# Performance work log

Hardware: AMD Instinct MI355X
Metric: run time of the kernel (lower is better)

The kernel has to match this reference:

```python
import jax, jax.numpy as jnp
import numpy as np

B, L_IN, D_MODEL, CONV_D, KSIZE = 16, 512, 384, 1536, 3
MEL_MAX = 4096
LN_EPS = 1e-5


def _conv1d_same(h, w, b):
    # h: [B, C_in, L], w: [C_out, C_in, K] -> [B, C_out, L]
    y = jax.lax.conv_general_dilated(h, w, window_strides=(1,), padding='SAME',
                                     dimension_numbers=('NCH', 'OIH', 'NCH'))
    return y + b[None, :, None]


def _layernorm(x, g, b):
    m = jnp.mean(x, -1, keepdims=True)
    v = jnp.mean((x - m) ** 2, -1, keepdims=True)
    return (x - m) * jax.lax.rsqrt(v + LN_EPS) * g + b


def _ffn(x, wa, ba, wb, bb):
    # Conv1D_FFT: conv(d_model->conv_d) ReLU conv(conv_d->d_model) ReLU
    h = jnp.transpose(x, (0, 2, 1))
    h = jax.nn.relu(_conv1d_same(h, wa, ba))
    h = jax.nn.relu(_conv1d_same(h, wb, bb))
    return jnp.transpose(h, (0, 2, 1))


def _dur_pred(x, w1, b1, w2, b2, g1, be1, w3, b3, w4, b4, g2, be2, wl, bl):
    h = _ffn(x, w1, b1, w2, b2)
    h = _layernorm(h, g1, be1)  # dropout is identity at eval
    h = _ffn(h, w3, b3, w4, b4)
    h = _layernorm(h, g2, be2)
    return (h @ wl + bl)[..., 0]  # [B, L_in], squeeze(-1)


def _length_regulate(x, dur, mel_max_len):
    # Equivalent to alignment @ x where alignment[b,t,j]=1 iff cum[b,j-1] <= t < cum[b,j],
    # padded with zeros out to mel_max_len (original pads output to mel_max_len).
    cum = jnp.cumsum(dur, axis=-1)                        # [B, L_in]
    total = cum[:, -1]                                    # [B]
    t = jnp.arange(mel_max_len, dtype=cum.dtype)          # [T]
    idx = jax.vmap(lambda c: jnp.searchsorted(c, t, side='right'))(cum)  # [B, T]
    idx = jnp.minimum(idx, x.shape[1] - 1)
    out = jnp.take_along_axis(x, idx[:, :, None], axis=1)  # [B, T, D]
    mask = (t[None, :] < total[:, None])[..., None]
    return out * mask


def setup_inputs() -> dict:
    key = jax.random.key(0)
    ks = jax.random.split(key, 8)
    def nrm(k, shape):
        return jax.random.normal(k, shape, jnp.float32) * 0.02
    return {
        'x': jax.random.normal(ks[0], (B, L_IN, D_MODEL), jnp.float32),
        'target': jax.random.randint(ks[1], (B, L_IN), 0, 8, jnp.int32),
        'mel_max_len': MEL_MAX,
        'w1': nrm(ks[2], (CONV_D, D_MODEL, KSIZE)), 'b1': jnp.zeros((CONV_D,), jnp.float32),
        'w2': nrm(ks[3], (D_MODEL, CONV_D, KSIZE)), 'b2': jnp.zeros((D_MODEL,), jnp.float32),
        'g1': jnp.ones((D_MODEL,), jnp.float32), 'be1': jnp.zeros((D_MODEL,), jnp.float32),
        'w3': nrm(ks[4], (CONV_D, D_MODEL, KSIZE)), 'b3': jnp.zeros((CONV_D,), jnp.float32),
        'w4': nrm(ks[5], (D_MODEL, CONV_D, KSIZE)), 'b4': jnp.zeros((D_MODEL,), jnp.float32),
        'g2': jnp.ones((D_MODEL,), jnp.float32), 'be2': jnp.zeros((D_MODEL,), jnp.float32),
        'wl': nrm(ks[6], (D_MODEL, 1)), 'bl': jnp.zeros((1,), jnp.float32),
    }


def reference(x, target, mel_max_len, w1, b1, w2, b2, g1, be1, w3, b3, w4, b4, g2, be2, wl, bl):
    dur_preds = _dur_pred(x, w1, b1, w2, b2, g1, be1, w3, b3, w4, b4, g2, be2, wl, bl)
    output = _length_regulate(x, target, mel_max_len)
    return (output, dur_preds)
```

## Files before the change

### kernel.cpp

```cpp
#include <hip/hip_runtime.h>
#include <hip/hip_bf16.h>
#include <cstddef>
#include <cstdint>

#define NB 16
#define LIN 512
#define DM 384
#define DC 1536
#define MELMAX 4096
#define LN_EPS 1e-5f

typedef __bf16 bf16x8 __attribute__((ext_vector_type(8)));
typedef float f32x4 __attribute__((ext_vector_type(4)));

#define GL2LDS(gp, lp)                                                                \
    __builtin_amdgcn_global_load_lds((const __attribute__((address_space(1))) void*)(gp), \
                                     (__attribute__((address_space(3))) void*)(lp), 16, 0, 0)

__device__ __forceinline__ float wred(float v) {
#pragma unroll
    for (int m = 32; m >= 1; m >>= 1) v += __shfl_xor(v, m, 64);
    return v;
}

__device__ __forceinline__ unsigned short f2bf(float f) {
    __hip_bfloat16 h = __float2bfloat16(f);
    return *reinterpret_cast<unsigned short*>(&h);
}

__device__ __forceinline__ float bf2f(unsigned short u) {
    return __uint_as_float(((unsigned)u) << 16);
}


__global__ void cumsum_kernel(const int* __restrict__ tgt, int* __restrict__ cum) {
    __shared__ int s[LIN];
    const int b = blockIdx.x, tid = threadIdx.x;
    s[tid] = tgt[b * LIN + tid];
    __syncthreads();
    for (int off = 1; off < LIN; off <<= 1) {
        int v = (tid >= off) ? s[tid - off] : 0;
        __syncthreads();
        s[tid] += v;
        __syncthreads();
    }
    cum[b * LIN + tid] = s[tid];
}


__global__ __launch_bounds__(256) void gather_kernel(const float* __restrict__ x,
                                                     const int* __restrict__ cum,
                                                     float* __restrict__ out) {
    const int wid = (blockIdx.x * 256 + threadIdx.x) >> 6;
    const int lane = threadIdx.x & 63;
    const int b = wid >> 12;
    const int t = wid & (MELMAX - 1);
    const int* c = cum + b * LIN;
    const int total = c[LIN - 1];
    float4* orow = reinterpret_cast<float4*>(out + ((size_t)b * MELMAX + t) * DM);
    if (t < total) {
        int lo = 0, hi = LIN;
        while (lo < hi) { int mid = (lo + hi) >> 1; if (c[mid] > t) hi = mid; else lo = mid + 1; }
        const int idx = lo < (LIN - 1) ? lo : (LIN - 1);
        const float4* xrow = reinterpret_cast<const float4*>(x + ((size_t)b * LIN + idx) * DM);
#pragma unroll
        for (int j = 0; j < 2; ++j) {
            const int p = lane + 64 * j;
            if (p < DM / 4) orow[p] = xrow[p];
        }
    } else {
        const float4 z = make_float4(0.f, 0.f, 0.f, 0.f);
#pragma unroll
        for (int j = 0; j < 2; ++j) {
            const int p = lane + 64 * j;
            if (p < DM / 4) orow[p] = z;
        }
    }
}


__global__ void zpad3_kernel(unsigned short* __restrict__ xb, unsigned short* __restrict__ hb,
                             unsigned short* __restrict__ h2) {
    const int i = blockIdx.x;
    const int buf = i >> 5, rem = i & 31;
    const int b = rem >> 1, row = (rem & 1) ? (LIN + 1) : 0;
    unsigned short* p = buf == 0 ? xb : (buf == 1 ? hb : h2);
    const int rl = buf == 1 ? DC : DM;
    unsigned short* base = p + ((size_t)b * (LIN + 2) + row) * rl;
    for (int c = threadIdx.x; c < rl; c += 256) base[c] = 0;
}

__global__ void cast_x_kernel(const float* __restrict__ x, unsigned short* __restrict__ xb) {
    const int idx = blockIdx.x * 256 + threadIdx.x;
    const int total = NB * LIN * DM / 4;
    if (idx >= total) return;
    const float4 v = reinterpret_cast<const float4*>(x)[idx];
    const int e = idx * 4;
    const int b = e / (LIN * DM);
    const int rem = e - b * (LIN * DM);
    const int l = rem / DM;
    const int c = rem - l * DM;
    ushort4 o;
    o.x = f2bf(v.x); o.y = f2bf(v.y); o.z = f2bf(v.z); o.w = f2bf(v.w);
    *reinterpret_cast<ushort4*>(xb + ((size_t)b * (LIN + 2) + l + 1) * DM + c) = o;
}

__global__ void wcast_all_kernel(const float* __restrict__ w1, const float* __restrict__ w2,
                                 const float* __restrict__ w3, const float* __restrict__ w4,
                                 unsigned short* __restrict__ o1, unsigned short* __restrict__ o2,
                                 unsigned short* __restrict__ o3, unsigned short* __restrict__ o4) {
    const int idx = blockIdx.x * 256 + threadIdx.x;
    if (idx >= DC * DM) return;
    const int which = blockIdx.y;
    const float* w = which == 0 ? w1 : which == 1 ? w2 : which == 2 ? w3 : w4;
    unsigned short* gg = which == 0 ? o1 : which == 1 ? o2 : which == 2 ? o3 : o4;
    const int CI = (which == 0 || which == 2) ? DM : DC;
    const int co = idx / CI, ci = idx - co * CI;
    const float* p = w + (size_t)idx * 3;
    unsigned short* o = gg + (size_t)co * (3 * CI) + ci;
    o[0 * CI] = f2bf(p[0]);
    o[1 * CI] = f2bf(p[1]);
    o[2 * CI] = f2bf(p[2]);
}


template <int CI, int CO, int BN>
__global__ __launch_bounds__(256, 2) void conv_mfma_kernel(const unsigned short* __restrict__ in,
                                                           const unsigned short* __restrict__ wg,
                                                           const float* __restrict__ bias,
                                                           unsigned short* __restrict__ out) {
    constexpr int BM = 128, BK = 32;
    constexpr int KC = CI / BK;
    constexpr int AROWS = BM + 16;
    constexpr int AGRP = AROWS / 16;
    constexpr int GPT = BN / 16;
    constexpr int BGRP = 3 * GPT;
    constexpr int NW_N = BN / 32;
    constexpr int NT = CO / BN;
    constexpr int MT = LIN / BM;

    __shared__ __align__(16) unsigned short As[2][AROWS * BK];
    __shared__ __align__(16) unsigned short Bs[2][3 * BN * BK];

    const int orig = blockIdx.x, nwg = gridDim.x;
    const int q = nwg >> 3, r = nwg & 7, xcd = orig & 7, o = orig >> 3;
    const int wgid = (xcd < r ? xcd * (q + 1) : r * (q + 1) + (xcd - r) * q) + o;

    const int mg = wgid / NT;
    const int nt = wgid - mg * NT;
    const int b = mg >> 2;
    const int l0 = (mg & (MT - 1)) * BM;
    const int n0 = nt * BN;

    const int tid = threadIdx.x;
    const int lane = tid & 63;
    const int wv = tid >> 6;
    const int wr = wv >> 1, wc = wv & 1;

    const unsigned short* inb = in + (size_t)b * (LIN + 2) * CI;

    f32x4 acc[4][NW_N];
#pragma unroll
    for (int m = 0; m < 4; ++m)
#pragma unroll
        for (int n = 0; n < NW_N; ++n) acc[m][n] = (f32x4){0.f, 0.f, 0.f, 0.f};

    const int lrow = lane >> 2;
    const int lch = lane & 3;
    const int fr = lane & 15, kg = lane >> 4;

    const unsigned short* aroot = inb + (size_t)l0 * CI + lch * 8;
    const unsigned short* broot = wg + (size_t)n0 * (3 * CI) + lch * 8;

#define STAGE(c, kb)                                                                      \
    do {                                                                                  \
        const unsigned short* abase = aroot + (kb) * BK;                                  \
        for (int g = wv; g < AGRP; g += 4)                                                \
            GL2LDS(abase + (size_t)(g * 16 + lrow) * CI, &As[c][g * 512]);                \
        const unsigned short* bbase = broot + (kb) * BK;                                  \
        for (int g2 = wv; g2 < BGRP; g2 += 4) {                                           \
            const int t = g2 / GPT, gr = g2 - t * GPT;                                    \
            GL2LDS(bbase + (size_t)(gr * 16 + lrow) * (3 * CI) + (size_t)t * CI,          \
                   &Bs[c][g2 * 512]);                                                     \
        }                                                                                 \
    } while (0)

#define COMPUTE(c)                                                                        \
    do {                                                                                  \
        _Pragma("unroll")                                                                 \
        for (int t = 0; t < 3; ++t) {                                                     \
            bf16x8 aF[4], bF[NW_N];                                                       \
            _Pragma("unroll")                                                             \
            for (int m = 0; m < 4; ++m)                                                   \
                aF[m] = *reinterpret_cast<const bf16x8*>(                                 \
                    &As[c][(t + wr * 64 + m * 16 + fr) * BK + kg * 8]);                   \
            _Pragma("unroll")                                                             \
            for (int n = 0; n < NW_N; ++n)                                                \
                bF[n] = *reinterpret_cast<const bf16x8*>(                                 \
                    &Bs[c][(t * BN + wc * (BN / 2) + n * 16 + fr) * BK + kg * 8]);        \
            _Pragma("unroll")                                                             \
            for (int m = 0; m < 4; ++m)                                                   \
                _Pragma("unroll")                                                         \
                for (int n = 0; n < NW_N; ++n)                                            \
                    acc[m][n] =                                                           \
                        __builtin_amdgcn_mfma_f32_16x16x32_bf16(aF[m], bF[n], acc[m][n],  \
                                                                0, 0, 0);                 \
        }                                                                                 \
    } while (0)

    STAGE(0, 0);
    __syncthreads();
#pragma unroll 1
    for (int kb = 0; kb < KC; kb += 2) {
        if (kb + 1 < KC) STAGE(1, kb + 1);
        COMPUTE(0);
        __syncthreads();
        if (kb + 2 < KC) STAGE(0, kb + 2);
        if (kb + 1 < KC) {
            COMPUTE(1);
            __syncthreads();
        }
    }
#undef STAGE
#undef COMPUTE

    const int fq = lane >> 4;
    float bv[NW_N];
#pragma unroll
    for (int n = 0; n < NW_N; ++n) bv[n] = bias[n0 + wc * (BN / 2) + n * 16 + fr];
    unsigned short* outb = out + (size_t)b * (LIN + 2) * CO;
#pragma unroll
    for (int m = 0; m < 4; ++m)
#pragma unroll
        for (int qy = 0; qy < 4; ++qy) {
            const int grow = l0 + wr * 64 + m * 16 + fq * 4 + qy + 1;
            unsigned short* orow = outb + (size_t)grow * CO + n0 + wc * (BN / 2) + fr;
#pragma unroll
            for (int n = 0; n < NW_N; ++n) {
                const float v = fmaxf(acc[m][n][qy] + bv[n], 0.f);
                orow[n * 16] = f2bf(v);
            }
        }
}


__global__ void ln_kernel(unsigned short* __restrict__ h, const float* __restrict__ g,
                          const float* __restrict__ be) {
    const int row = blockIdx.x, lane = threadIdx.x;
    const int b = row >> 9, l = row & (LIN - 1);
    unsigned short* hr = h + ((size_t)b * (LIN + 2) + l + 1) * DM;
    float v[6];
    float s = 0.f;
#pragma unroll
    for (int j = 0; j < 6; ++j) { v[j] = bf2f(hr[lane + 64 * j]); s += v[j]; }
    s = wred(s);
    const float mean = s * (1.f / DM);
    float vs = 0.f;
#pragma unroll
    for (int j = 0; j < 6; ++j) { const float d = v[j] - mean; vs += d * d; }
    vs = wred(vs);
    const float rstd = rsqrtf(vs * (1.f / DM) + LN_EPS);
#pragma unroll
    for (int j = 0; j < 6; ++j) {
        const int c = lane + 64 * j;
        hr[c] = f2bf((v[j] - mean) * rstd * g[c] + be[c]);
    }
}


__global__ void ln_linear_kernel(const unsigned short* __restrict__ h, const float* __restrict__ g,
                                 const float* __restrict__ be, const float* __restrict__ wl,
                                 const float* __restrict__ bl, float* __restrict__ dur) {
    const int row = blockIdx.x, lane = threadIdx.x;
    const int b = row >> 9, l = row & (LIN - 1);
    const unsigned short* hr = h + ((size_t)b * (LIN + 2) + l + 1) * DM;
    float v[6];
    float s = 0.f;
#pragma unroll
    for (int j = 0; j < 6; ++j) { v[j] = bf2f(hr[lane + 64 * j]); s += v[j]; }
    s = wred(s);
    const float mean = s * (1.f / DM);
    float vs = 0.f;
#pragma unroll
    for (int j = 0; j < 6; ++j) { const float d = v[j] - mean; vs += d * d; }
    vs = wred(vs);
    const float rstd = rsqrtf(vs * (1.f / DM) + LN_EPS);
    float dot = 0.f;
#pragma unroll
    for (int j = 0; j < 6; ++j) {
        const int c = lane + 64 * j;
        dot += ((v[j] - mean) * rstd * g[c] + be[c]) * wl[c];
    }
    dot = wred(dot);
    if (lane == 0) dur[row] = dot + bl[0];
}


extern "C" void kernel_launch(void* const* d_in, const int* in_sizes, int n_in,
                              void* d_out, int out_size, void* d_ws, size_t ws_size,
                              hipStream_t stream) {
    const float* x   = (const float*)d_in[0];
    const int*   tgt = (const int*)d_in[1];
    const float* w1  = (const float*)d_in[3];
    const float* b1  = (const float*)d_in[4];
    const float* w2  = (const float*)d_in[5];
    const float* b2  = (const float*)d_in[6];
    const float* g1  = (const float*)d_in[7];
    const float* be1 = (const float*)d_in[8];
    const float* w3  = (const float*)d_in[9];
    const float* b3  = (const float*)d_in[10];
    const float* w4  = (const float*)d_in[11];
    const float* b4  = (const float*)d_in[12];
    const float* g2  = (const float*)d_in[13];
    const float* be2 = (const float*)d_in[14];
    const float* wl  = (const float*)d_in[15];
    const float* bl  = (const float*)d_in[16];

    float* out = (float*)d_out;
    float* dur = out + (size_t)NB * MELMAX * DM;

    unsigned short* ws = (unsigned short*)d_ws;
    unsigned short* xb   = ws;
    unsigned short* hbig = xb + (size_t)NB * (LIN + 2) * DM;
    unsigned short* h2b  = hbig + (size_t)NB * (LIN + 2) * DC;
    unsigned short* wg1  = h2b + (size_t)NB * (LIN + 2) * DM;
    unsigned short* wg2  = wg1 + (size_t)DC * 3 * DM;
    unsigned short* wg3  = wg2 + (size_t)DM * 3 * DC;
    unsigned short* wg4  = wg3 + (size_t)DC * 3 * DM;
    int* cum = (int*)(wg4 + (size_t)DM * 3 * DC);

    cumsum_kernel<<<NB, LIN, 0, stream>>>(tgt, cum);
    gather_kernel<<<(NB * MELMAX) / 4, 256, 0, stream>>>(x, cum, out);

    zpad3_kernel<<<NB * 2 * 3, 256, 0, stream>>>(xb, hbig, h2b);
    cast_x_kernel<<<(NB * LIN * DM / 4 + 255) / 256, 256, 0, stream>>>(x, xb);
    wcast_all_kernel<<<dim3((DC * DM + 255) / 256, 4), 256, 0, stream>>>(w1, w2, w3, w4,
                                                                         wg1, wg2, wg3, wg4);

    conv_mfma_kernel<DM, DC, 128><<<NB * (LIN / 128) * (DC / 128), 256, 0, stream>>>(xb, wg1, b1, hbig);
    conv_mfma_kernel<DC, DM, 64><<<NB * (LIN / 128) * (DM / 64), 256, 0, stream>>>(hbig, wg2, b2, h2b);
    ln_kernel<<<NB * LIN, 64, 0, stream>>>(h2b, g1, be1);
    conv_mfma_kernel<DM, DC, 128><<<NB * (LIN / 128) * (DC / 128), 256, 0, stream>>>(h2b, wg3, b3, hbig);
    conv_mfma_kernel<DC, DM, 64><<<NB * (LIN / 128) * (DM / 64), 256, 0, stream>>>(hbig, wg4, b4, xb);
    ln_linear_kernel<<<NB * LIN, 64, 0, stream>>>(xb, g2, be2, wl, bl, dur);
}
```

Before: 231.9 us.

## Read conv weights directly from global, merge prep kernels, fuse gather into first conv

The weight (B) operand of the conv MFMA kernel is no longer staged through LDS. Each lane loads its bf16x8 weight fragments straight from global memory, which removes the B shared buffer and frees LDS so occupancy can rise to 3 blocks per CU. The zero-pad, x-cast and weight-cast kernels are merged into one prep launch, and the length-regulator gather blocks are appended to the first conv grid so both run inside one dispatch. The cost is uncoalesced, L2-dependent global weight loads inside the inner loop. The XCD remap also now assumes the conv block count divides evenly by 8.

```diff
diff --git a/kernel.cpp b/kernel.cpp
--- a/kernel.cpp
+++ b/kernel.cpp
@@ -48,70 +48,42 @@
 }
 
 
-__global__ __launch_bounds__(256) void gather_kernel(const float* __restrict__ x,
-                                                     const int* __restrict__ cum,
-                                                     float* __restrict__ out) {
-    const int wid = (blockIdx.x * 256 + threadIdx.x) >> 6;
-    const int lane = threadIdx.x & 63;
-    const int b = wid >> 12;
-    const int t = wid & (MELMAX - 1);
-    const int* c = cum + b * LIN;
-    const int total = c[LIN - 1];
-    float4* orow = reinterpret_cast<float4*>(out + ((size_t)b * MELMAX + t) * DM);
-    if (t < total) {
-        int lo = 0, hi = LIN;
-        while (lo < hi) { int mid = (lo + hi) >> 1; if (c[mid] > t) hi = mid; else lo = mid + 1; }
-        const int idx = lo < (LIN - 1) ? lo : (LIN - 1);
-        const float4* xrow = reinterpret_cast<const float4*>(x + ((size_t)b * LIN + idx) * DM);
-#pragma unroll
-        for (int j = 0; j < 2; ++j) {
-            const int p = lane + 64 * j;
-            if (p < DM / 4) orow[p] = xrow[p];
-        }
-    } else {
-        const float4 z = make_float4(0.f, 0.f, 0.f, 0.f);
-#pragma unroll
-        for (int j = 0; j < 2; ++j) {
-            const int p = lane + 64 * j;
-            if (p < DM / 4) orow[p] = z;
-        }
-    }
-}
-
-
-__global__ void zpad3_kernel(unsigned short* __restrict__ xb, unsigned short* __restrict__ hb,
-                             unsigned short* __restrict__ h2) {
-    const int i = blockIdx.x;
-    const int buf = i >> 5, rem = i & 31;
-    const int b = rem >> 1, row = (rem & 1) ? (LIN + 1) : 0;
-    unsigned short* p = buf == 0 ? xb : (buf == 1 ? hb : h2);
-    const int rl = buf == 1 ? DC : DM;
-    unsigned short* base = p + ((size_t)b * (LIN + 2) + row) * rl;
-    for (int c = threadIdx.x; c < rl; c += 256) base[c] = 0;
-}
-
-__global__ void cast_x_kernel(const float* __restrict__ x, unsigned short* __restrict__ xb) {
-    const int idx = blockIdx.x * 256 + threadIdx.x;
-    const int total = NB * LIN * DM / 4;
-    if (idx >= total) return;
-    const float4 v = reinterpret_cast<const float4*>(x)[idx];
-    const int e = idx * 4;
-    const int b = e / (LIN * DM);
-    const int rem = e - b * (LIN * DM);
-    const int l = rem / DM;
-    const int c = rem - l * DM;
-    ushort4 o;
-    o.x = f2bf(v.x); o.y = f2bf(v.y); o.z = f2bf(v.z); o.w = f2bf(v.w);
-    *reinterpret_cast<ushort4*>(xb + ((size_t)b * (LIN + 2) + l + 1) * DM + c) = o;
-}
-
-__global__ void wcast_all_kernel(const float* __restrict__ w1, const float* __restrict__ w2,
-                                 const float* __restrict__ w3, const float* __restrict__ w4,
-                                 unsigned short* __restrict__ o1, unsigned short* __restrict__ o2,
-                                 unsigned short* __restrict__ o3, unsigned short* __restrict__ o4) {
-    const int idx = blockIdx.x * 256 + threadIdx.x;
-    if (idx >= DC * DM) return;
-    const int which = blockIdx.y;
+#define ZPAD_BLKS 96
+#define CASTX_BLKS 3072
+#define WCAST_BLKS 2304
+
+__global__ void prep_kernel(const float* __restrict__ x, unsigned short* __restrict__ xb,
+                            unsigned short* __restrict__ hbig, unsigned short* __restrict__ h2b,
+                            const float* __restrict__ w1, const float* __restrict__ w2,
+                            const float* __restrict__ w3, const float* __restrict__ w4,
+                            unsigned short* __restrict__ o1, unsigned short* __restrict__ o2,
+                            unsigned short* __restrict__ o3, unsigned short* __restrict__ o4) {
+    const int bid = blockIdx.x, tid = threadIdx.x;
+    if (bid < ZPAD_BLKS) {
+        const int buf = bid >> 5, rem = bid & 31;
+        const int b = rem >> 1, row = (rem & 1) ? (LIN + 1) : 0;
+        unsigned short* p = buf == 0 ? xb : (buf == 1 ? hbig : h2b);
+        const int rl = buf == 1 ? DC : DM;
+        unsigned short* base = p + ((size_t)b * (LIN + 2) + row) * rl;
+        for (int c = tid; c < rl; c += 256) base[c] = 0;
+        return;
+    }
+    if (bid < ZPAD_BLKS + CASTX_BLKS) {
+        const int idx = (bid - ZPAD_BLKS) * 256 + tid;
+        const float4 v = reinterpret_cast<const float4*>(x)[idx];
+        const int e = idx * 4;
+        const int b = e / (LIN * DM);
+        const int rem = e - b * (LIN * DM);
+        const int l = rem / DM;
+        const int c = rem - l * DM;
+        ushort4 o;
+        o.x = f2bf(v.x); o.y = f2bf(v.y); o.z = f2bf(v.z); o.w = f2bf(v.w);
+        *reinterpret_cast<ushort4*>(xb + ((size_t)b * (LIN + 2) + l + 1) * DM + c) = o;
+        return;
+    }
+    const int j = bid - ZPAD_BLKS - CASTX_BLKS;
+    const int which = j / WCAST_BLKS;
+    const int idx = (j - which * WCAST_BLKS) * 256 + tid;
     const float* w = which == 0 ? w1 : which == 1 ? w2 : which == 2 ? w3 : w4;
     unsigned short* gg = which == 0 ? o1 : which == 1 ? o2 : which == 2 ? o3 : o4;
     const int CI = (which == 0 || which == 2) ? DM : DC;
@@ -124,37 +96,66 @@
 }
 
 
-template <int CI, int CO, int BN>
-__global__ __launch_bounds__(256, 2) void conv_mfma_kernel(const unsigned short* __restrict__ in,
+template <int CI, int CO, int BN, bool FUSE>
+__global__ __launch_bounds__(256, 3) void conv_mfma_kernel(const unsigned short* __restrict__ in,
                                                            const unsigned short* __restrict__ wg,
                                                            const float* __restrict__ bias,
-                                                           unsigned short* __restrict__ out) {
+                                                           unsigned short* __restrict__ out,
+                                                           const float* __restrict__ xf,
+                                                           const int* __restrict__ cum,
+                                                           float* __restrict__ gout) {
     constexpr int BM = 128, BK = 32;
     constexpr int KC = CI / BK;
     constexpr int AROWS = BM + 16;
     constexpr int AGRP = AROWS / 16;
-    constexpr int GPT = BN / 16;
-    constexpr int BGRP = 3 * GPT;
     constexpr int NW_N = BN / 32;
     constexpr int NT = CO / BN;
-    constexpr int MT = LIN / BM;
+    constexpr int NCONV = NB * (LIN / BM) * NT;
 
     __shared__ __align__(16) unsigned short As[2][AROWS * BK];
-    __shared__ __align__(16) unsigned short Bs[2][3 * BN * BK];
-
-    const int orig = blockIdx.x, nwg = gridDim.x;
-    const int q = nwg >> 3, r = nwg & 7, xcd = orig & 7, o = orig >> 3;
-    const int wgid = (xcd < r ? xcd * (q + 1) : r * (q + 1) + (xcd - r) * q) + o;
+
+    const int tid = threadIdx.x;
+    const int lane = tid & 63;
+    const int wv = tid >> 6;
+
+    if (FUSE && blockIdx.x >= NCONV) {
+        const int wid = (blockIdx.x - NCONV) * 4 + wv;
+        const int b = wid >> 12;
+        const int t = wid & (MELMAX - 1);
+        const int* c = cum + b * LIN;
+        const int total = c[LIN - 1];
+        float4* orow = reinterpret_cast<float4*>(gout + ((size_t)b * MELMAX + t) * DM);
+        if (t < total) {
+            int lo = 0, hi = LIN;
+            while (lo < hi) { int mid = (lo + hi) >> 1; if (c[mid] > t) hi = mid; else lo = mid + 1; }
+            const int idx = lo < (LIN - 1) ? lo : (LIN - 1);
+            const float4* xrow = reinterpret_cast<const float4*>(xf + ((size_t)b * LIN + idx) * DM);
+#pragma unroll
+            for (int j = 0; j < 2; ++j) {
+                const int p = lane + 64 * j;
+                if (p < DM / 4) orow[p] = xrow[p];
+            }
+        } else {
+            const float4 z = make_float4(0.f, 0.f, 0.f, 0.f);
+#pragma unroll
+            for (int j = 0; j < 2; ++j) {
+                const int p = lane + 64 * j;
+                if (p < DM / 4) orow[p] = z;
+            }
+        }
+        return;
+    }
+
+    const int orig = blockIdx.x;
+    const int q = NCONV >> 3, xcd = orig & 7, o = orig >> 3;
+    const int wgid = xcd * q + o;
 
     const int mg = wgid / NT;
     const int nt = wgid - mg * NT;
     const int b = mg >> 2;
-    const int l0 = (mg & (MT - 1)) * BM;
+    const int l0 = (mg & 3) * BM;
     const int n0 = nt * BN;
 
-    const int tid = threadIdx.x;
-    const int lane = tid & 63;
-    const int wv = tid >> 6;
     const int wr = wv >> 1, wc = wv & 1;
 
     const unsigned short* inb = in + (size_t)b * (LIN + 2) * CI;
@@ -170,41 +171,38 @@
     const int fr = lane & 15, kg = lane >> 4;
 
     const unsigned short* aroot = inb + (size_t)l0 * CI + lch * 8;
-    const unsigned short* broot = wg + (size_t)n0 * (3 * CI) + lch * 8;
+    const unsigned short* bfrag = wg + (size_t)(n0 + wc * (BN / 2) + fr) * (3 * CI) + kg * 8;
 
 #define STAGE(c, kb)                                                                      \
     do {                                                                                  \
         const unsigned short* abase = aroot + (kb) * BK;                                  \
         for (int g = wv; g < AGRP; g += 4)                                                \
             GL2LDS(abase + (size_t)(g * 16 + lrow) * CI, &As[c][g * 512]);                \
-        const unsigned short* bbase = broot + (kb) * BK;                                  \
-        for (int g2 = wv; g2 < BGRP; g2 += 4) {                                           \
-            const int t = g2 / GPT, gr = g2 - t * GPT;                                    \
-            GL2LDS(bbase + (size_t)(gr * 16 + lrow) * (3 * CI) + (size_t)t * CI,          \
-                   &Bs[c][g2 * 512]);                                                     \
-        }                                                                                 \
     } while (0)
 
-#define COMPUTE(c)                                                                        \
+#define COMPUTE(c, kb)                                                                    \
     do {                                                                                  \
+        bf16x8 bF[3][NW_N];                                                               \
+        _Pragma("unroll")                                                                 \
+        for (int t = 0; t < 3; ++t)                                                       \
+            _Pragma("unroll")                                                             \
+            for (int n = 0; n < NW_N; ++n)                                                \
+                bF[t][n] = *reinterpret_cast<const bf16x8*>(                              \
+                    bfrag + (size_t)(n * 16) * (3 * CI) + t * CI + (kb) * BK);            \
         _Pragma("unroll")                                                                 \
         for (int t = 0; t < 3; ++t) {                                                     \
-            bf16x8 aF[4], bF[NW_N];                                                       \
+            bf16x8 aF[4];                                                                 \
             _Pragma("unroll")                                                             \
             for (int m = 0; m < 4; ++m)                                                   \
                 aF[m] = *reinterpret_cast<const bf16x8*>(                                 \
                     &As[c][(t + wr * 64 + m * 16 + fr) * BK + kg * 8]);                   \
             _Pragma("unroll")                                                             \
-            for (int n = 0; n < NW_N; ++n)                                                \
-                bF[n] = *reinterpret_cast<const bf16x8*>(                                 \
-                    &Bs[c][(t * BN + wc * (BN / 2) + n * 16 + fr) * BK + kg * 8]);        \
-            _Pragma("unroll")                                                             \
             for (int m = 0; m < 4; ++m)                                                   \
                 _Pragma("unroll")                                                         \
                 for (int n = 0; n < NW_N; ++n)                                            \
                     acc[m][n] =                                                           \
-                        __builtin_amdgcn_mfma_f32_16x16x32_bf16(aF[m], bF[n], acc[m][n],  \
-                                                                0, 0, 0);                 \
+                        __builtin_amdgcn_mfma_f32_16x16x32_bf16(aF[m], bF[t][n],          \
+                                                                acc[m][n], 0, 0, 0);      \
         }                                                                                 \
     } while (0)
 
@@ -213,11 +211,11 @@
 #pragma unroll 1
     for (int kb = 0; kb < KC; kb += 2) {
         if (kb + 1 < KC) STAGE(1, kb + 1);
-        COMPUTE(0);
+        COMPUTE(0, kb);
         __syncthreads();
         if (kb + 2 < KC) STAGE(0, kb + 2);
         if (kb + 1 < KC) {
-            COMPUTE(1);
+            COMPUTE(1, kb + 1);
             __syncthreads();
         }
     }
@@ -330,17 +328,20 @@
     int* cum = (int*)(wg4 + (size_t)DM * 3 * DC);
 
     cumsum_kernel<<<NB, LIN, 0, stream>>>(tgt, cum);
-    gather_kernel<<<(NB * MELMAX) / 4, 256, 0, stream>>>(x, cum, out);
-
-    zpad3_kernel<<<NB * 2 * 3, 256, 0, stream>>>(xb, hbig, h2b);
-    cast_x_kernel<<<(NB * LIN * DM / 4 + 255) / 256, 256, 0, stream>>>(x, xb);
-    wcast_all_kernel<<<dim3((DC * DM + 255) / 256, 4), 256, 0, stream>>>(w1, w2, w3, w4,
-                                                                         wg1, wg2, wg3, wg4);
-
-    conv_mfma_kernel<DM, DC, 128><<<NB * (LIN / 128) * (DC / 128), 256, 0, stream>>>(xb, wg1, b1, hbig);
-    conv_mfma_kernel<DC, DM, 64><<<NB * (LIN / 128) * (DM / 64), 256, 0, stream>>>(hbig, wg2, b2, h2b);
+    prep_kernel<<<ZPAD_BLKS + CASTX_BLKS + 4 * WCAST_BLKS, 256, 0, stream>>>(
+        x, xb, hbig, h2b, w1, w2, w3, w4, wg1, wg2, wg3, wg4);
+
+    const int NCONV1 = NB * (LIN / 128) * (DC / 128);
+    const int NGATH = (NB * MELMAX) / 4;
+    conv_mfma_kernel<DM, DC, 128, true><<<NCONV1 + NGATH, 256, 0, stream>>>(
+        xb, wg1, b1, hbig, x, cum, out);
+
+    conv_mfma_kernel<DC, DM, 64, false><<<NB * (LIN / 128) * (DM / 64), 256, 0, stream>>>(
+        hbig, wg2, b2, h2b, nullptr, nullptr, nullptr);
     ln_kernel<<<NB * LIN, 64, 0, stream>>>(h2b, g1, be1);
-    conv_mfma_kernel<DM, DC, 128><<<NB * (LIN / 128) * (DC / 128), 256, 0, stream>>>(h2b, wg3, b3, hbig);
-    conv_mfma_kernel<DC, DM, 64><<<NB * (LIN / 128) * (DM / 64), 256, 0, stream>>>(hbig, wg4, b4, xb);
+    conv_mfma_kernel<DM, DC, 128, false><<<NB * (LIN / 128) * (DC / 128), 256, 0, stream>>>(
+        h2b, wg3, b3, hbig, nullptr, nullptr, nullptr);
+    conv_mfma_kernel<DC, DM, 64, false><<<NB * (LIN / 128) * (DM / 64), 256, 0, stream>>>(
+        hbig, wg4, b4, xb, nullptr, nullptr, nullptr);
     ln_linear_kernel<<<NB * LIN, 64, 0, stream>>>(xb, g2, be2, wl, bl, dur);
 }
```

Measured after the change: 320.6 us. 1.38x slower.
